# Kernel tuning notes

Hardware: AMD Instinct MI355X
Metric: run time of the kernel (lower is better)

The kernel has to match this reference:

```python
import jax, jax.numpy as jnp
import numpy as np

B, T, K, H = 256, 64, 49, 512


def setup_inputs() -> dict:
    key = jax.random.key(0)
    ks = jax.random.split(key, 7)
    s = 0.02
    return {
        "V": jax.random.normal(ks[0], (B, K, H), dtype=jnp.float32),
        "h_t": jax.random.normal(ks[1], (B, T, H), dtype=jnp.float32),
        "s_t": jax.random.normal(ks[2], (B, T, H), dtype=jnp.float32),
        "Wv": jax.random.normal(ks[3], (K, H), dtype=jnp.float32) * s,  # affine_v.weight [49, hidden]
        "Wg": jax.random.normal(ks[4], (K, H), dtype=jnp.float32) * s,  # affine_g.weight
        "Ws": jax.random.normal(ks[5], (K, H), dtype=jnp.float32) * s,  # affine_s.weight
        "Wh": jax.random.normal(ks[6], (1, K), dtype=jnp.float32) * s,  # affine_h.weight [1, 49]
    }


def reference(V, h_t, s_t, Wv, Wg, Ws, Wh):
    # Dropout is identity (inference / eval mode).
    content_v = jnp.einsum('bkh,ah->bka', V, Wv)      # [B,K,49]
    content_g = jnp.einsum('bth,ah->bta', h_t, Wg)    # [B,T,49]
    # broadcast add -> [B,T,K,49], tanh, project 49->1
    z_t = jnp.einsum('btka,a->btk',
                     jnp.tanh(content_g[:, :, None, :] + content_v[:, None, :, :]),
                     Wh[0])                            # [B,T,K]
    alpha_t = jax.nn.softmax(z_t, axis=-1)             # softmax over K regions
    c_t = jnp.einsum('btk,bkh->bth', alpha_t, V)       # [B,T,H]
    content_s = jnp.einsum('bth,ah->bta', s_t, Ws) + content_g  # [B,T,49]
    z_ext = jnp.einsum('bta,a->bt', jnp.tanh(content_s), Wh[0])[:, :, None]  # [B,T,1]
    extended = jnp.concatenate([z_t, z_ext], axis=2)   # [B,T,K+1]
    alpha_hat = jax.nn.softmax(extended, axis=-1)
    beta_t = alpha_hat[:, :, -1:]                      # [B,T,1] sentinel gate
    c_hat_t = beta_t * s_t + (1.0 - beta_t) * c_t      # [B,T,H]
    return (c_hat_t, alpha_t, beta_t)
```

## Files before the change

kernel.cpp:

```cpp
#include <hip/hip_runtime.h>
#include <hip/hip_bf16.h>
#include <math.h>

#define Bn 256
#define Tn 64
#define Kn 49
#define Hn 512
#define An 49

#define WS_EV 0
#define WS_EG 614656
#define WS_ES 1417472

#define OUT_ALPHA 8388608
#define OUT_BETA  9191424

typedef __attribute__((ext_vector_type(8))) short short8;
typedef __attribute__((ext_vector_type(4))) short short4v;
typedef __attribute__((ext_vector_type(4))) float f32x4;

#define WLDS 520

__device__ __forceinline__ short bfc(float x) {
    __hip_bfloat16 h = __float2bfloat16(x);
    return __builtin_bit_cast(short, h);
}

__global__ __launch_bounds__(256) void gemm3_mfma(
    const float* __restrict__ V, const float* __restrict__ h_t,
    const float* __restrict__ s_t, const float* __restrict__ Wv,
    const float* __restrict__ Wg, const float* __restrict__ Ws,
    float* __restrict__ ws)
{
    const int b = blockIdx.x;
    const int part = blockIdx.y;

    const float* A;
    const float* W;
    float* out;
    int R;
    if (part == 0)      { A = V   + (size_t)b*Kn*Hn; W = Wv; out = ws + WS_EV + (size_t)b*Kn*An; R = Kn; }
    else if (part == 1) { A = h_t + (size_t)b*Tn*Hn; W = Wg; out = ws + WS_EG + (size_t)b*Tn*An; R = Tn; }
    else                { A = s_t + (size_t)b*Tn*Hn; W = Ws; out = ws + WS_ES + (size_t)b*Tn*An; R = Tn; }

    __shared__ short Wl[Kn * WLDS];

    const int tid = threadIdx.x;

    for (int i = tid; i < Kn * 128; i += 256) {
        const int row = i >> 7;
        const int c4  = (i & 127) << 2;
        float4 v = *(const float4*)(W + (size_t)row * Hn + c4);
        short4v s;
        s.x = bfc(v.x); s.y = bfc(v.y); s.z = bfc(v.z); s.w = bfc(v.w);
        *(short4v*)(&Wl[row * WLDS + c4]) = s;
    }
    __syncthreads();

    const int wave = tid >> 6;
    const int lane = tid & 63;
    const int l15  = lane & 15;
    const int kgrp = lane >> 4;
    const int koff = kgrp * 8;

    const int r0 = wave * 16;
    int arow = r0 + l15; if (arow >= R) arow = R - 1;
    const float* Ap = A + (size_t)arow * Hn + koff;

    int brow[4];
    #pragma unroll
    for (int ct = 0; ct < 4; ++ct) {
        int r = ct * 16 + l15;
        brow[ct] = (r < Kn) ? r : (Kn - 1);
    }

    f32x4 acc[4] = {{0,0,0,0},{0,0,0,0},{0,0,0,0},{0,0,0,0}};

    for (int ks = 0; ks < 16; ++ks) {
        float4 a0 = *(const float4*)(Ap + ks * 32);
        float4 a1 = *(const float4*)(Ap + ks * 32 + 4);
        short8 af;
        af[0] = bfc(a0.x); af[1] = bfc(a0.y); af[2] = bfc(a0.z); af[3] = bfc(a0.w);
        af[4] = bfc(a1.x); af[5] = bfc(a1.y); af[6] = bfc(a1.z); af[7] = bfc(a1.w);
        #pragma unroll
        for (int ct = 0; ct < 4; ++ct) {
            short8 bfr = *(const short8*)(&Wl[brow[ct] * WLDS + koff + ks * 32]);
            acc[ct] = __builtin_amdgcn_mfma_f32_16x16x32_bf16(af, bfr, acc[ct], 0, 0, 0);
        }
    }

    #pragma unroll
    for (int ct = 0; ct < 4; ++ct) {
        const int a = ct * 16 + l15;
        if (a >= An) continue;
        #pragma unroll
        for (int i = 0; i < 4; ++i) {
            const int k = r0 + kgrp * 4 + i;
            if (k < R) out[(size_t)k * An + a] = __expf(2.0f * acc[ct][i]);
        }
    }
}

#define TT 16
#define AP 52

__global__ __launch_bounds__(256) void fused_kernel(
    const float* __restrict__ V, const float* __restrict__ s_t,
    const float* __restrict__ Wh, const float* __restrict__ ws,
    float* __restrict__ out)
{
    const int bid = blockIdx.x;
    const int b  = bid >> 2;
    const int t0 = (bid & 3) * TT;

    __shared__ float EvL[Kn * AP];
    __shared__ float EgL[TT * AP];
    __shared__ float EcL[TT * AP];
    __shared__ float whL[AP];
    __shared__ float zl[TT][Kn + 1];
    __shared__ float al[TT][AP];
    __shared__ float bl[TT];
    __shared__ float swhL;

    const int tid = threadIdx.x;

    {
        const float* evg = ws + WS_EV + (size_t)b * Kn * An;
        for (int i = tid; i < Kn * An; i += 256) {
            const int r = i / An;
            const int c = i - r * An;
            EvL[r * AP + c] = evg[i];
        }
        const float* egg = ws + WS_EG + ((size_t)b * Tn + t0) * An;
        const float* esg = ws + WS_ES + ((size_t)b * Tn + t0) * An;
        for (int i = tid; i < TT * An; i += 256) {
            const int r = i / An;
            const int c = i - r * An;
            const float eg = egg[i];
            EgL[r * AP + c] = eg;
            EcL[r * AP + c] = eg * esg[i];
        }
        if (tid < Kn * 3) {
            const int r = tid / 3;
            const int c = An + (tid - r * 3);
            EvL[r * AP + c] = 1.f;
        }
        if (tid >= 64 && tid < 64 + TT * 3) {
            const int j = tid - 64;
            const int r = j / 3;
            const int c = An + (j - r * 3);
            EgL[r * AP + c] = 1.f;
            EcL[r * AP + c] = 1.f;
        }
        float whv = 0.f;
        if (tid < AP) { whv = (tid < An) ? Wh[tid] : 0.f; whL[tid] = whv; }
        if (tid < 64) {
            float sv = whv;
            #pragma unroll
            for (int o = 32; o; o >>= 1) sv += __shfl_xor(sv, o, 64);
            if (tid == 0) swhL = sv;
        }
    }
    __syncthreads();

    const float swh = swhL;

    for (int idx = tid; idx < TT * Kn + TT; idx += 256) {
        if (idx < TT * Kn) {
            const int tt = idx / Kn;
            const int k  = idx - tt * Kn;
            const float4* eg4 = (const float4*)&EgL[tt * AP];
            const float4* ev4 = (const float4*)&EvL[k * AP];
            const float4* wh4 = (const float4*)whL;
            float acc = 0.f;
            #pragma unroll
            for (int j = 0; j < 13; ++j) {
                const float4 g = eg4[j], v = ev4[j], w = wh4[j];
                acc += w.x * __builtin_amdgcn_rcpf(g.x * v.x + 1.f);
                acc += w.y * __builtin_amdgcn_rcpf(g.y * v.y + 1.f);
                acc += w.z * __builtin_amdgcn_rcpf(g.z * v.z + 1.f);
                acc += w.w * __builtin_amdgcn_rcpf(g.w * v.w + 1.f);
            }
            zl[tt][k] = swh - 2.f * acc;
        } else {
            const int tt = idx - TT * Kn;
            const float4* ec4 = (const float4*)&EcL[tt * AP];
            const float4* wh4 = (const float4*)whL;
            float acc = 0.f;
            #pragma unroll
            for (int j = 0; j < 13; ++j) {
                const float4 c = ec4[j], w = wh4[j];
                acc += w.x * __builtin_amdgcn_rcpf(c.x + 1.f);
                acc += w.y * __builtin_amdgcn_rcpf(c.y + 1.f);
                acc += w.z * __builtin_amdgcn_rcpf(c.z + 1.f);
                acc += w.w * __builtin_amdgcn_rcpf(c.w + 1.f);
            }
            zl[tt][Kn] = swh - 2.f * acc;
        }
    }
    __syncthreads();

    {
        const int w    = tid >> 6;
        const int lane = tid & 63;
        #pragma unroll
        for (int rr = 0; rr < 4; ++rr) {
            const int row = w * 4 + rr;
            float v = (lane < Kn) ? zl[row][lane] : -1e30f;
            float m = v;
            #pragma unroll
            for (int o = 32; o; o >>= 1) m = fmaxf(m, __shfl_xor(m, o, 64));
            float e = (lane < Kn) ? __expf(v - m) : 0.f;
            float s = e;
            #pragma unroll
            for (int o = 32; o; o >>= 1) s += __shfl_xor(s, o, 64);
            const float ze  = zl[row][Kn];
            const float m2  = fmaxf(m, ze);
            const float eze = __expf(ze - m2);
            const float denom = s * __expf(m - m2) + eze;
            const float beta  = eze * __builtin_amdgcn_rcpf(denom);
            const float a = e * __builtin_amdgcn_rcpf(s);
            if (lane < AP) al[row][lane] = a;
            if (lane < Kn)
                out[OUT_ALPHA + ((size_t)(b * Tn + t0 + row)) * Kn + lane] = a;
            if (lane == 0) {
                bl[row] = beta;
                out[OUT_BETA + (b * Tn + t0 + row)] = beta;
            }
        }
    }
    __syncthreads();

    {
        const float2* vb2 = (const float2*)(V + (size_t)b * Kn * Hn);
        float2 acc2[TT];
        #pragma unroll
        for (int r = 0; r < TT; ++r) { acc2[r].x = 0.f; acc2[r].y = 0.f; }

        for (int j = 0; j < 13; ++j) {
            const int k0 = j * 4;
            float2 vv[4];
            #pragma unroll
            for (int u = 0; u < 4; ++u) {
                int kk = k0 + u; kk = (kk > Kn - 1) ? (Kn - 1) : kk;
                vv[u] = vb2[(size_t)kk * (Hn / 2) + tid];
            }
            #pragma unroll
            for (int r = 0; r < TT; ++r) {
                const float4 a4 = *(const float4*)&al[r][k0];
                acc2[r].x += a4.x * vv[0].x + a4.y * vv[1].x + a4.z * vv[2].x + a4.w * vv[3].x;
                acc2[r].y += a4.x * vv[0].y + a4.y * vv[1].y + a4.z * vv[2].y + a4.w * vv[3].y;
            }
        }

        #pragma unroll
        for (int r = 0; r < TT; ++r) {
            const float beta = bl[r];
            const float omb  = 1.f - beta;
            const size_t row = (size_t)(b * Tn + t0 + r) * Hn;
            const float2 sv = *(const float2*)(s_t + row + 2 * tid);
            float2 o;
            o.x = beta * sv.x + omb * acc2[r].x;
            o.y = beta * sv.y + omb * acc2[r].y;
            *(float2*)(out + row + 2 * tid) = o;
        }
    }
}

extern "C" void kernel_launch(void* const* d_in, const int* in_sizes, int n_in,
                              void* d_out, int out_size, void* d_ws, size_t ws_size,
                              hipStream_t stream)
{
    const float* V   = (const float*)d_in[0];
    const float* h_t = (const float*)d_in[1];
    const float* s_t = (const float*)d_in[2];
    const float* Wv  = (const float*)d_in[3];
    const float* Wg  = (const float*)d_in[4];
    const float* Ws  = (const float*)d_in[5];
    const float* Wh  = (const float*)d_in[6];
    float* out = (float*)d_out;
    float* ws  = (float*)d_ws;

    dim3 g1(Bn, 3);
    gemm3_mfma<<<g1, 256, 0, stream>>>(V, h_t, s_t, Wv, Wg, Ws, ws);
    fused_kernel<<<Bn * 4, 256, 0, stream>>>(V, s_t, Wh, ws, out);
}
```

Before: 175.2 us.

## Pre-convert weights to bf16 MFMA fragment layout in a separate prep kernel

Adds a small prep kernel that converts Wv/Wg/Ws to bf16 once and stores them in the workspace already arranged in per-lane MFMA B-fragment order. The GEMM kernel then reads B fragments directly from global memory (cached in L2) instead of every block converting the full weight matrix into LDS and synchronising. This removes redundant per-block conversion and the LDS footprint, which may raise occupancy. The costs are an extra kernel launch and global/L2 reads in the inner loop in place of LDS reads.

Measured after the change: 175.6 us. No clear change (+0.2%).

```diff
diff --git a/kernel.cpp b/kernel.cpp
--- a/kernel.cpp
+++ b/kernel.cpp
@@ -11,52 +11,62 @@
 #define WS_EV 0
 #define WS_EG 614656
 #define WS_ES 1417472
+#define WS_WF 2220288
 
 #define OUT_ALPHA 8388608
 #define OUT_BETA  9191424
 
 typedef __attribute__((ext_vector_type(8))) short short8;
-typedef __attribute__((ext_vector_type(4))) short short4v;
 typedef __attribute__((ext_vector_type(4))) float f32x4;
-
-#define WLDS 520
 
 __device__ __forceinline__ short bfc(float x) {
     __hip_bfloat16 h = __float2bfloat16(x);
     return __builtin_bit_cast(short, h);
 }
 
+__global__ __launch_bounds__(256) void prep_w(
+    const float* __restrict__ Wv, const float* __restrict__ Wg,
+    const float* __restrict__ Ws, float* __restrict__ ws)
+{
+    const int tid = blockIdx.x * 256 + threadIdx.x;
+    const int part = tid >> 12;
+    const int rem  = tid & 4095;
+    const int lane = rem & 63;
+    const int ks   = (rem >> 6) & 15;
+    const int ct   = rem >> 10;
+    const int row  = ct * 16 + (lane & 15);
+    const int k0   = (lane >> 4) * 8 + ks * 32;
+    const float* W = (part == 0) ? Wv : (part == 1) ? Wg : Ws;
+
+    short8 s;
+    #pragma unroll
+    for (int j = 0; j < 8; ++j) s[j] = 0;
+    if (row < Kn) {
+        float4 v0 = *(const float4*)(W + (size_t)row * Hn + k0);
+        float4 v1 = *(const float4*)(W + (size_t)row * Hn + k0 + 4);
+        s[0] = bfc(v0.x); s[1] = bfc(v0.y); s[2] = bfc(v0.z); s[3] = bfc(v0.w);
+        s[4] = bfc(v1.x); s[5] = bfc(v1.y); s[6] = bfc(v1.z); s[7] = bfc(v1.w);
+    }
+    ((short8*)((short*)(ws + WS_WF)))[tid] = s;
+}
+
 __global__ __launch_bounds__(256) void gemm3_mfma(
     const float* __restrict__ V, const float* __restrict__ h_t,
-    const float* __restrict__ s_t, const float* __restrict__ Wv,
-    const float* __restrict__ Wg, const float* __restrict__ Ws,
-    float* __restrict__ ws)
+    const float* __restrict__ s_t, float* __restrict__ ws)
 {
     const int b = blockIdx.x;
     const int part = blockIdx.y;
 
     const float* A;
-    const float* W;
     float* out;
     int R;
-    if (part == 0)      { A = V   + (size_t)b*Kn*Hn; W = Wv; out = ws + WS_EV + (size_t)b*Kn*An; R = Kn; }
-    else if (part == 1) { A = h_t + (size_t)b*Tn*Hn; W = Wg; out = ws + WS_EG + (size_t)b*Tn*An; R = Tn; }
-    else                { A = s_t + (size_t)b*Tn*Hn; W = Ws; out = ws + WS_ES + (size_t)b*Tn*An; R = Tn; }
-
-    __shared__ short Wl[Kn * WLDS];
-
-    const int tid = threadIdx.x;
-
-    for (int i = tid; i < Kn * 128; i += 256) {
-        const int row = i >> 7;
-        const int c4  = (i & 127) << 2;
-        float4 v = *(const float4*)(W + (size_t)row * Hn + c4);
-        short4v s;
-        s.x = bfc(v.x); s.y = bfc(v.y); s.z = bfc(v.z); s.w = bfc(v.w);
-        *(short4v*)(&Wl[row * WLDS + c4]) = s;
-    }
-    __syncthreads();
-
+    if (part == 0)      { A = V   + (size_t)b*Kn*Hn; out = ws + WS_EV + (size_t)b*Kn*An; R = Kn; }
+    else if (part == 1) { A = h_t + (size_t)b*Tn*Hn; out = ws + WS_EG + (size_t)b*Tn*An; R = Tn; }
+    else                { A = s_t + (size_t)b*Tn*Hn; out = ws + WS_ES + (size_t)b*Tn*An; R = Tn; }
+
+    const short8* wf = (const short8*)((const short*)(ws + WS_WF)) + (size_t)part * 4096;
+
+    const int tid  = threadIdx.x;
     const int wave = tid >> 6;
     const int lane = tid & 63;
     const int l15  = lane & 15;
@@ -67,26 +77,20 @@
     int arow = r0 + l15; if (arow >= R) arow = R - 1;
     const float* Ap = A + (size_t)arow * Hn + koff;
 
-    int brow[4];
-    #pragma unroll
-    for (int ct = 0; ct < 4; ++ct) {
-        int r = ct * 16 + l15;
-        brow[ct] = (r < Kn) ? r : (Kn - 1);
-    }
-
     f32x4 acc[4] = {{0,0,0,0},{0,0,0,0},{0,0,0,0},{0,0,0,0}};
 
+    #pragma unroll 4
     for (int ks = 0; ks < 16; ++ks) {
         float4 a0 = *(const float4*)(Ap + ks * 32);
         float4 a1 = *(const float4*)(Ap + ks * 32 + 4);
         short8 af;
         af[0] = bfc(a0.x); af[1] = bfc(a0.y); af[2] = bfc(a0.z); af[3] = bfc(a0.w);
         af[4] = bfc(a1.x); af[5] = bfc(a1.y); af[6] = bfc(a1.z); af[7] = bfc(a1.w);
-        #pragma unroll
-        for (int ct = 0; ct < 4; ++ct) {
-            short8 bfr = *(const short8*)(&Wl[brow[ct] * WLDS + koff + ks * 32]);
-            acc[ct] = __builtin_amdgcn_mfma_f32_16x16x32_bf16(af, bfr, acc[ct], 0, 0, 0);
-        }
+        const short8* wp = wf + ks * 64 + lane;
+        acc[0] = __builtin_amdgcn_mfma_f32_16x16x32_bf16(af, wp[0],       acc[0], 0, 0, 0);
+        acc[1] = __builtin_amdgcn_mfma_f32_16x16x32_bf16(af, wp[16 * 64], acc[1], 0, 0, 0);
+        acc[2] = __builtin_amdgcn_mfma_f32_16x16x32_bf16(af, wp[32 * 64], acc[2], 0, 0, 0);
+        acc[3] = __builtin_amdgcn_mfma_f32_16x16x32_bf16(af, wp[48 * 64], acc[3], 0, 0, 0);
     }
 
     #pragma unroll
@@ -281,7 +285,8 @@
     float* out = (float*)d_out;
     float* ws  = (float*)d_ws;
 
+    prep_w<<<48, 256, 0, stream>>>(Wv, Wg, Ws, ws);
     dim3 g1(Bn, 3);
-    gemm3_mfma<<<g1, 256, 0, stream>>>(V, h_t, s_t, Wv, Wg, Ws, ws);
+    gemm3_mfma<<<g1, 256, 0, stream>>>(V, h_t, s_t, ws);
     fused_kernel<<<Bn * 4, 256, 0, stream>>>(V, s_t, Wh, ws, out);
 }
```
